# Kernel optimization log

Hardware: AMD Instinct MI355X
Metric: run time of the kernel (lower is better)

## Reference

```python
import jax, jax.numpy as jnp
import numpy as np

B, H, W, F, D = 8, 126, 126, 64, 32
ITERS, NIT = 3, 20
RHO, NU, DT, FRC = 1.0, 0.1, 0.1, 1.0
DX = 2.0 / (B + 1)
DY = 2.0 / (H + 1)
DX2, DY2 = DX * DX, DY * DY
DEN = 2.0 * (DX2 + DY2)


def _b_term(du_dx, dv_dy, du_dy, dv_dx):
    return RHO * ((du_dx + dv_dy) / DT - du_dx**2 - 2.0 * du_dy * dv_dx - dv_dy**2)


def build_b(u, v):
    b = jnp.zeros_like(u)
    # interior
    b = b.at[:, 1:-1, 1:-1].set(_b_term(
        (u[:, 1:-1, 2:] - u[:, 1:-1, :-2]) / (2 * DX),
        (v[:, 2:, 1:-1] - v[:, :-2, 1:-1]) / (2 * DY),
        (u[:, 2:, 1:-1] - u[:, :-2, 1:-1]) / (2 * DY),
        (v[:, 1:-1, 2:] - v[:, 1:-1, :-2]) / (2 * DX)))
    # periodic wrap, last column
    b = b.at[:, 1:-1, -1].set(_b_term(
        (u[:, 1:-1, 0] - u[:, 1:-1, -2]) / (2 * DX),
        (v[:, 2:, -1] - v[:, :-2, -1]) / (2 * DY),
        (u[:, 2:, -1] - u[:, :-2, -1]) / (2 * DY),
        (v[:, 1:-1, 0] - v[:, 1:-1, -2]) / (2 * DX)))
    # periodic wrap, first column
    b = b.at[:, 1:-1, 0].set(_b_term(
        (u[:, 1:-1, 1] - u[:, 1:-1, -1]) / (2 * DX),
        (v[:, 2:, 0] - v[:, :-2, 0]) / (2 * DY),
        (u[:, 2:, 0] - u[:, :-2, 0]) / (2 * DY),
        (v[:, 1:-1, 1] - v[:, 1:-1, -1]) / (2 * DX)))
    return b


def pressure_poisson(p, b):
    c = DX2 * DY2 / DEN

    def step(p, _):
        pn = p
        p = p.at[:, 1:-1, 1:-1].set(
            ((pn[:, 1:-1, 2:] + pn[:, 1:-1, :-2]) * DY2 + (pn[:, 2:, 1:-1] + pn[:, :-2, 1:-1]) * DX2) / DEN
            - c * b[:, 1:-1, 1:-1])
        p = p.at[:, 1:-1, -1].set(
            ((pn[:, 1:-1, 0] + pn[:, 1:-1, -2]) * DY2 + (pn[:, 2:, -1] + pn[:, :-2, -1]) * DX2) / DEN
            - c * b[:, 1:-1, -1])
        p = p.at[:, 1:-1, 0].set(
            ((pn[:, 1:-1, 1] + pn[:, 1:-1, -1]) * DY2 + (pn[:, 2:, 0] + pn[:, :-2, 0]) * DX2) / DEN
            - c * b[:, 1:-1, 0])
        # Neumann-style row boundaries (copy from updated p, as in torch code)
        p = p.at[:, -1].set(p[:, -2])
        p = p.at[:, 0].set(p[:, 1])
        return p, None

    p, _ = jax.lax.scan(step, p, None, length=NIT)
    return p


def velocity_step(u, v, p):
    un, vn = u, v
    uc = un[:, 1:-1, 1:-1]
    vc = vn[:, 1:-1, 1:-1]
    u_i = (uc - uc * DT / DX * (uc - un[:, 1:-1, :-2]) - vc * DT / DY * (uc - un[:, :-2, 1:-1])
           - DT / (2 * RHO * DX) * (p[:, 1:-1, 2:] - p[:, 1:-1, :-2])
           + NU * (DT / DX2 * (un[:, 1:-1, 2:] - 2 * uc + un[:, 1:-1, :-2])
                   + DT / DY2 * (un[:, 2:, 1:-1] - 2 * uc + un[:, :-2, 1:-1]))
           + FRC * DT)
    v_i = (vc - uc * DT / DX * (vc - vn[:, 1:-1, :-2]) - vc * DT / DY * (vc - vn[:, :-2, 1:-1])
           - DT / (2 * RHO * DY) * (p[:, 2:, 1:-1] - p[:, :-2, 1:-1])
           + NU * (DT / DX2 * (vn[:, 1:-1, 2:] - 2 * vc + vn[:, 1:-1, :-2])
                   + DT / DY2 * (vn[:, 2:, 1:-1] - 2 * vc + vn[:, :-2, 1:-1])))
    ue = un[:, 1:-1, -1]
    ve = vn[:, 1:-1, -1]
    u_e = (ue - ue * DT / DX * (ue - un[:, 1:-1, -2]) - ve * DT / DY * (ue - un[:, :-2, -1])
           - DT / (2 * RHO * DX) * (p[:, 1:-1, 0] - p[:, 1:-1, -2])
           + NU * (DT / DX2 * (un[:, 1:-1, 0] - 2 * ue + un[:, 1:-1, -2])
                   + DT / DY2 * (un[:, 2:, -1] - 2 * ue + un[:, :-2, -1]))
           + FRC * DT)
    v_e = (ve - ue * DT / DX * (ve - vn[:, 1:-1, -2]) - ve * DT / DY * (ve - vn[:, :-2, -1])
           - DT / (2 * RHO * DY) * (p[:, 2:, -1] - p[:, :-2, -1])
           + NU * (DT / DX2 * (vn[:, 1:-1, 0] - 2 * ve + vn[:, 1:-1, -2])
                   + DT / DY2 * (vn[:, 2:, -1] - 2 * ve + vn[:, :-2, -1])))
    u0c = un[:, 1:-1, 0]
    v0c = vn[:, 1:-1, 0]
    u_0 = (u0c - u0c * DT / DX * (u0c - un[:, 1:-1, -1]) - v0c * DT / DY * (u0c - un[:, :-2, 0])
           - DT / (2 * RHO * DX) * (p[:, 1:-1, 1] - p[:, 1:-1, -1])
           + NU * (DT / DX2 * (un[:, 1:-1, 1] - 2 * u0c + un[:, 1:-1, -1])
                   + DT / DY2 * (un[:, 2:, 0] - 2 * u0c + un[:, :-2, 0]))
           + FRC * DT)
    v_0 = (v0c - u0c * DT / DX * (v0c - vn[:, 1:-1, -1]) - v0c * DT / DY * (v0c - vn[:, :-2, 0])
           - DT / (2 * RHO * DY) * (p[:, 2:, 0] - p[:, :-2, 0])
           + NU * (DT / DX2 * (vn[:, 1:-1, 1] - 2 * v0c + vn[:, 1:-1, -1])
                   + DT / DY2 * (vn[:, 2:, 0] - 2 * v0c + vn[:, :-2, 0])))
    u = un.at[:, 1:-1, 1:-1].set(u_i).at[:, 1:-1, -1].set(u_e).at[:, 1:-1, 0].set(u_0)
    v = vn.at[:, 1:-1, 1:-1].set(v_i).at[:, 1:-1, -1].set(v_e).at[:, 1:-1, 0].set(v_0)
    u = u.at[:, 0].set(0.0).at[:, -1].set(0.0)
    v = v.at[:, 0].set(0.0).at[:, -1].set(0.0)
    return u, v


def setup_inputs() -> dict:
    key = jax.random.key(0)
    ks = jax.random.split(key, 5)
    x = jax.random.normal(ks[0], (B, H, W, F), jnp.float32) * 0.05
    u0 = jax.random.normal(ks[1], (B, H + 2, W + 2, D), jnp.float32) * 0.05
    v0 = jax.random.normal(ks[2], (B, H + 2, W + 2, D), jnp.float32) * 0.05
    w = jax.random.normal(ks[3], (D, F), jnp.float32) / np.float32(np.sqrt(F))
    b_lin = jax.random.normal(ks[4], (D,), jnp.float32) * 0.01
    return {"x": x, "u0": u0, "v0": v0, "w": w, "b_lin": b_lin}


def reference(x, u0, v0, w, b_lin):
    # pad spatial dims by 1 then linear preprocess: (B,H+2,W+2,F) -> (B,H+2,W+2,D)
    p = jnp.pad(x, ((0, 0), (1, 1), (1, 1), (0, 0)))
    p = jnp.einsum('bhwf,df->bhwd', p, w) + b_lin
    u, v = u0, v0
    for _ in range(ITERS):
        b = build_b(u, v)
        p = pressure_poisson(p, b)
        u, v = velocity_step(u, v, p)
    return p[:, -1, :, :]  # (B, W+2, D)
```

## Files before the change

### kernel.cpp

```cpp
#include <hip/hip_runtime.h>

#define NITER 20
#define OUTER 3

constexpr double DXd  = 2.0 / 9.0;
constexpr double DYd  = 2.0 / 127.0;
constexpr double DX2d = DXd * DXd;
constexpr double DY2d = DYd * DYd;
constexpr double DENd = 2.0 * (DX2d + DY2d);

constexpr float K1     = (float)(DY2d / DENd);
constexpr float K2     = (float)(DX2d / DENd);
constexpr float CC     = (float)(DX2d * DY2d / DENd);
constexpr float INV2DX = (float)(1.0 / (2.0 * DXd));
constexpr float INV2DY = (float)(1.0 / (2.0 * DYd));
constexpr float INVDT  = (float)(1.0 / 0.1);
constexpr float DTDX   = (float)(0.1 / DXd);
constexpr float DTDY   = (float)(0.1 / DYd);
constexpr float PGX    = (float)(0.1 / (2.0 * 1.0 * DXd));
constexpr float PGY    = (float)(0.1 / (2.0 * 1.0 * DYd));
constexpr float A1     = (float)(0.1 / DX2d);
constexpr float A2     = (float)(0.1 / DY2d);
constexpr float NUf    = 0.1f;
constexpr float FDT    = 0.1f;

#define ROR1(x)  __int_as_float(__builtin_amdgcn_mov_dpp(__float_as_int(x), 0x121, 0xF, 0xF, false))
#define ROR15(x) __int_as_float(__builtin_amdgcn_mov_dpp(__float_as_int(x), 0x12F, 0xF, 0xF, false))
#define FROM_LO(x) (selLower ? ROR1(x) : ROR15(x))
#define FROM_HI(x) (selLower ? ROR15(x) : ROR1(x))

__global__ __launch_bounds__(256) void einsum_kernel(
    const float* __restrict__ x, const float* __restrict__ w,
    const float* __restrict__ bl, float* __restrict__ p0)
{
    int id = blockIdx.x * 256 + threadIdx.x;
    int c = id & 127, r = (id >> 7) & 127, b = id >> 14;
    float acc[32];
#pragma unroll
    for (int d = 0; d < 32; ++d) acc[d] = bl[d];
    if (r >= 1 && r <= 126 && c >= 1 && c <= 126) {
        const float* xp = x + (((size_t)(b * 126 + (r - 1))) * 126 + (c - 1)) * 64;
#pragma unroll
        for (int f = 0; f < 64; f += 4) {
            float4 xv = *(const float4*)(xp + f);
#pragma unroll
            for (int d = 0; d < 32; ++d) {
                acc[d] += xv.x * w[d * 64 + f] + xv.y * w[d * 64 + f + 1]
                        + xv.z * w[d * 64 + f + 2] + xv.w * w[d * 64 + f + 3];
            }
        }
    }
    float* op = p0 + ((size_t)b * 32) * 16384 + r * 128 + c;
#pragma unroll
    for (int d = 0; d < 32; ++d) op[(size_t)d * 16384] = acc[d];
}

__global__ __launch_bounds__(512, 2) void sim_kernel(
    const float* __restrict__ u0, const float* __restrict__ v0,
    const float* __restrict__ p0ws, const float* __restrict__ x,
    const float* __restrict__ w, const float* __restrict__ bl,
    float* __restrict__ out, int use_ws)
{
    __shared__ float sP[2][32][2][128];
    __shared__ float sU[32][2][128];
    __shared__ float sV[32][2][128];

    const int tid = threadIdx.x;
    const int tx = tid & 15, ty = tid >> 4;
    const int c0 = tx << 3, r0 = ty << 2;
    const int lane = tid & 63;
    const int bb = blockIdx.x & 7;
    const int d  = blockIdx.x >> 3;
    const int tyN = (ty > 0) ? ty - 1 : 0;
    const int tyS = (ty < 31) ? ty + 1 : 31;

    const int pr = __builtin_amdgcn_mov_dpp(lane, 0x121, 0xF, 0xF, false);
    const bool selLower = (pr == ((lane & 48) | ((lane + 15) & 15)));

    float pC[4][8], uC[4][8], vC[4][8], cb[4][8];

#pragma unroll
    for (int r = 0; r < 4; ++r) {
        const size_t base = ((size_t)((bb * 128 + (r0 + r)) * 128 + c0)) * 32 + d;
#pragma unroll
        for (int c = 0; c < 8; ++c) {
            uC[r][c] = u0[base + (size_t)c * 32];
            vC[r][c] = v0[base + (size_t)c * 32];
        }
    }

    if (use_ws) {
        const float* pp = p0ws + ((size_t)(bb * 32 + d)) * 16384;
#pragma unroll
        for (int r = 0; r < 4; ++r) {
            float4 a = *(const float4*)(pp + (r0 + r) * 128 + c0);
            float4 b = *(const float4*)(pp + (r0 + r) * 128 + c0 + 4);
            pC[r][0] = a.x; pC[r][1] = a.y; pC[r][2] = a.z; pC[r][3] = a.w;
            pC[r][4] = b.x; pC[r][5] = b.y; pC[r][6] = b.z; pC[r][7] = b.w;
        }
    } else {
        const float blv = bl[d];
#pragma unroll
        for (int r = 0; r < 4; ++r) {
            const int gr = r0 + r;
#pragma unroll
            for (int c = 0; c < 8; ++c) {
                const int gc = c0 + c;
                float acc = blv;
                if (gr >= 1 && gr <= 126 && gc >= 1 && gc <= 126) {
                    const float* xp = x + (((size_t)(bb * 126 + (gr - 1))) * 126 + (gc - 1)) * 64;
                    for (int f = 0; f < 64; f += 4) {
                        float4 xv = *(const float4*)(xp + f);
                        acc += xv.x * w[d * 64 + f] + xv.y * w[d * 64 + f + 1]
                             + xv.z * w[d * 64 + f + 2] + xv.w * w[d * 64 + f + 3];
                    }
                }
                pC[r][c] = acc;
            }
        }
    }

    int s = 0;
    *(float4*)&sP[0][ty][0][c0]     = make_float4(pC[0][0], pC[0][1], pC[0][2], pC[0][3]);
    *(float4*)&sP[0][ty][0][c0 + 4] = make_float4(pC[0][4], pC[0][5], pC[0][6], pC[0][7]);
    *(float4*)&sP[0][ty][1][c0]     = make_float4(pC[3][0], pC[3][1], pC[3][2], pC[3][3]);
    *(float4*)&sP[0][ty][1][c0 + 4] = make_float4(pC[3][4], pC[3][5], pC[3][6], pC[3][7]);
    *(float4*)&sU[ty][0][c0]        = make_float4(uC[0][0], uC[0][1], uC[0][2], uC[0][3]);
    *(float4*)&sU[ty][0][c0 + 4]    = make_float4(uC[0][4], uC[0][5], uC[0][6], uC[0][7]);
    *(float4*)&sU[ty][1][c0]        = make_float4(uC[3][0], uC[3][1], uC[3][2], uC[3][3]);
    *(float4*)&sU[ty][1][c0 + 4]    = make_float4(uC[3][4], uC[3][5], uC[3][6], uC[3][7]);
    *(float4*)&sV[ty][0][c0]        = make_float4(vC[0][0], vC[0][1], vC[0][2], vC[0][3]);
    *(float4*)&sV[ty][0][c0 + 4]    = make_float4(vC[0][4], vC[0][5], vC[0][6], vC[0][7]);
    *(float4*)&sV[ty][1][c0]        = make_float4(vC[3][0], vC[3][1], vC[3][2], vC[3][3]);
    *(float4*)&sV[ty][1][c0 + 4]    = make_float4(vC[3][4], vC[3][5], vC[3][6], vC[3][7]);
    __syncthreads();

    for (int outer = 0; outer < OUTER; ++outer) {
        {
            float uNh[8], uSh[8], vNh[8], vSh[8];
            {
                float4 a, b;
                a = *(const float4*)&sU[tyN][1][c0]; b = *(const float4*)&sU[tyN][1][c0 + 4];
                uNh[0]=a.x; uNh[1]=a.y; uNh[2]=a.z; uNh[3]=a.w; uNh[4]=b.x; uNh[5]=b.y; uNh[6]=b.z; uNh[7]=b.w;
                a = *(const float4*)&sU[tyS][0][c0]; b = *(const float4*)&sU[tyS][0][c0 + 4];
                uSh[0]=a.x; uSh[1]=a.y; uSh[2]=a.z; uSh[3]=a.w; uSh[4]=b.x; uSh[5]=b.y; uSh[6]=b.z; uSh[7]=b.w;
                a = *(const float4*)&sV[tyN][1][c0]; b = *(const float4*)&sV[tyN][1][c0 + 4];
                vNh[0]=a.x; vNh[1]=a.y; vNh[2]=a.z; vNh[3]=a.w; vNh[4]=b.x; vNh[5]=b.y; vNh[6]=b.z; vNh[7]=b.w;
                a = *(const float4*)&sV[tyS][0][c0]; b = *(const float4*)&sV[tyS][0][c0 + 4];
                vSh[0]=a.x; vSh[1]=a.y; vSh[2]=a.z; vSh[3]=a.w; vSh[4]=b.x; vSh[5]=b.y; vSh[6]=b.z; vSh[7]=b.w;
            }
#pragma unroll
            for (int r = 0; r < 4; ++r) {
                float uWh = FROM_LO(uC[r][7]);
                float uEh = FROM_HI(uC[r][0]);
                float vWh = FROM_LO(vC[r][7]);
                float vEh = FROM_HI(vC[r][0]);
#pragma unroll
                for (int c = 0; c < 8; ++c) {
                    float uE = (c < 7) ? uC[r][c + 1] : uEh;
                    float uW = (c > 0) ? uC[r][c - 1] : uWh;
                    float vE = (c < 7) ? vC[r][c + 1] : vEh;
                    float vW = (c > 0) ? vC[r][c - 1] : vWh;
                    float uN = (r > 0) ? uC[r - 1][c] : uNh[c];
                    float uS = (r < 3) ? uC[r + 1][c] : uSh[c];
                    float vN = (r > 0) ? vC[r - 1][c] : vNh[c];
                    float vS = (r < 3) ? vC[r + 1][c] : vSh[c];
                    float dudx = (uE - uW) * INV2DX;
                    float dvdy = (vS - vN) * INV2DY;
                    float dudy = (uS - uN) * INV2DY;
                    float dvdx = (vE - vW) * INV2DX;
                    float bt = (dudx + dvdy) * INVDT - dudx * dudx
                             - 2.0f * dudy * dvdx - dvdy * dvdy;
                    cb[r][c] = CC * bt;
                }
            }
        }

        for (int it = 0; it < NITER; ++it) {
            float nrow[8], shalo[8];
            {
                float4 a, b;
                a = *(const float4*)&sP[s][tyN][1][c0]; b = *(const float4*)&sP[s][tyN][1][c0 + 4];
                nrow[0]=a.x; nrow[1]=a.y; nrow[2]=a.z; nrow[3]=a.w; nrow[4]=b.x; nrow[5]=b.y; nrow[6]=b.z; nrow[7]=b.w;
                a = *(const float4*)&sP[s][tyS][0][c0]; b = *(const float4*)&sP[s][tyS][0][c0 + 4];
                shalo[0]=a.x; shalo[1]=a.y; shalo[2]=a.z; shalo[3]=a.w; shalo[4]=b.x; shalo[5]=b.y; shalo[6]=b.z; shalo[7]=b.w;
            }
#pragma unroll
            for (int r = 0; r < 4; ++r) {
                float old0[8];
#pragma unroll
                for (int c = 0; c < 8; ++c) old0[c] = pC[r][c];
                float pWh = FROM_LO(old0[7]);
                float pEh = FROM_HI(old0[0]);
#pragma unroll
                for (int c = 0; c < 8; ++c) {
                    float E = (c < 7) ? old0[c + 1] : pEh;
                    float W = (c > 0) ? old0[c - 1] : pWh;
                    float N = nrow[c];
                    float S = (r < 3) ? pC[r + 1][c] : shalo[c];
                    pC[r][c] = (E + W) * K1 + (N + S) * K2 - cb[r][c];
                }
#pragma unroll
                for (int c = 0; c < 8; ++c) nrow[c] = old0[c];
            }
            if (ty == 0) {
#pragma unroll
                for (int c = 0; c < 8; ++c) pC[0][c] = pC[1][c];
            }
            if (ty == 31) {
#pragma unroll
                for (int c = 0; c < 8; ++c) pC[3][c] = pC[2][c];
            }
            *(float4*)&sP[s ^ 1][ty][0][c0]     = make_float4(pC[0][0], pC[0][1], pC[0][2], pC[0][3]);
            *(float4*)&sP[s ^ 1][ty][0][c0 + 4] = make_float4(pC[0][4], pC[0][5], pC[0][6], pC[0][7]);
            *(float4*)&sP[s ^ 1][ty][1][c0]     = make_float4(pC[3][0], pC[3][1], pC[3][2], pC[3][3]);
            *(float4*)&sP[s ^ 1][ty][1][c0 + 4] = make_float4(pC[3][4], pC[3][5], pC[3][6], pC[3][7]);
            __syncthreads();
            s ^= 1;
        }

        if (outer < OUTER - 1) {
            float uNh[8], uSh[8], vNh[8], vSh[8], pNh[8], pSh[8];
            {
                float4 a, b;
                a = *(const float4*)&sU[tyN][1][c0]; b = *(const float4*)&sU[tyN][1][c0 + 4];
                uNh[0]=a.x; uNh[1]=a.y; uNh[2]=a.z; uNh[3]=a.w; uNh[4]=b.x; uNh[5]=b.y; uNh[6]=b.z; uNh[7]=b.w;
                a = *(const float4*)&sU[tyS][0][c0]; b = *(const float4*)&sU[tyS][0][c0 + 4];
                uSh[0]=a.x; uSh[1]=a.y; uSh[2]=a.z; uSh[3]=a.w; uSh[4]=b.x; uSh[5]=b.y; uSh[6]=b.z; uSh[7]=b.w;
                a = *(const float4*)&sV[tyN][1][c0]; b = *(const float4*)&sV[tyN][1][c0 + 4];
                vNh[0]=a.x; vNh[1]=a.y; vNh[2]=a.z; vNh[3]=a.w; vNh[4]=b.x; vNh[5]=b.y; vNh[6]=b.z; vNh[7]=b.w;
                a = *(const float4*)&sV[tyS][0][c0]; b = *(const float4*)&sV[tyS][0][c0 + 4];
                vSh[0]=a.x; vSh[1]=a.y; vSh[2]=a.z; vSh[3]=a.w; vSh[4]=b.x; vSh[5]=b.y; vSh[6]=b.z; vSh[7]=b.w;
                a = *(const float4*)&sP[s][tyN][1][c0]; b = *(const float4*)&sP[s][tyN][1][c0 + 4];
                pNh[0]=a.x; pNh[1]=a.y; pNh[2]=a.z; pNh[3]=a.w; pNh[4]=b.x; pNh[5]=b.y; pNh[6]=b.z; pNh[7]=b.w;
                a = *(const float4*)&sP[s][tyS][0][c0]; b = *(const float4*)&sP[s][tyS][0][c0 + 4];
                pSh[0]=a.x; pSh[1]=a.y; pSh[2]=a.z; pSh[3]=a.w; pSh[4]=b.x; pSh[5]=b.y; pSh[6]=b.z; pSh[7]=b.w;
            }
            __syncthreads();

            float uNrow[8], vNrow[8];
#pragma unroll
            for (int c = 0; c < 8; ++c) { uNrow[c] = uNh[c]; vNrow[c] = vNh[c]; }
#pragma unroll
            for (int r = 0; r < 4; ++r) {
                float uold[8], vold[8];
#pragma unroll
                for (int c = 0; c < 8; ++c) { uold[c] = uC[r][c]; vold[c] = vC[r][c]; }
                float uWh = FROM_LO(uold[7]);
                float uEh = FROM_HI(uold[0]);
                float vWh = FROM_LO(vold[7]);
                float vEh = FROM_HI(vold[0]);
                float pWh = FROM_LO(pC[r][7]);
                float pEh = FROM_HI(pC[r][0]);
#pragma unroll
                for (int c = 0; c < 8; ++c) {
                    float uc = uold[c], vc = vold[c];
                    float uE = (c < 7) ? uold[c + 1] : uEh;
                    float uW = (c > 0) ? uold[c - 1] : uWh;
                    float vE = (c < 7) ? vold[c + 1] : vEh;
                    float vW = (c > 0) ? vold[c - 1] : vWh;
                    float uN = uNrow[c];
                    float uS = (r < 3) ? uC[r + 1][c] : uSh[c];
                    float vN = vNrow[c];
                    float vS = (r < 3) ? vC[r + 1][c] : vSh[c];
                    float pE = (c < 7) ? pC[r][c + 1] : pEh;
                    float pW = (c > 0) ? pC[r][c - 1] : pWh;
                    float pN = (r > 0) ? pC[r - 1][c] : pNh[c];
                    float pS = (r < 3) ? pC[r + 1][c] : pSh[c];

                    float unew = uc - uc * DTDX * (uc - uW) - vc * DTDY * (uc - uN)
                               - PGX * (pE - pW)
                               + NUf * (A1 * (uE - 2.0f * uc + uW) + A2 * (uS - 2.0f * uc + uN))
                               + FDT;
                    float vnew = vc - uc * DTDX * (vc - vW) - vc * DTDY * (vc - vN)
                               - PGY * (pS - pN)
                               + NUf * (A1 * (vE - 2.0f * vc + vW) + A2 * (vS - 2.0f * vc + vN));
                    uC[r][c] = unew;
                    vC[r][c] = vnew;
                }
#pragma unroll
                for (int c = 0; c < 8; ++c) { uNrow[c] = uold[c]; vNrow[c] = vold[c]; }
            }
            if (ty == 0) {
#pragma unroll
                for (int c = 0; c < 8; ++c) { uC[0][c] = 0.0f; vC[0][c] = 0.0f; }
            }
            if (ty == 31) {
#pragma unroll
                for (int c = 0; c < 8; ++c) { uC[3][c] = 0.0f; vC[3][c] = 0.0f; }
            }
            *(float4*)&sU[ty][0][c0]     = make_float4(uC[0][0], uC[0][1], uC[0][2], uC[0][3]);
            *(float4*)&sU[ty][0][c0 + 4] = make_float4(uC[0][4], uC[0][5], uC[0][6], uC[0][7]);
            *(float4*)&sU[ty][1][c0]     = make_float4(uC[3][0], uC[3][1], uC[3][2], uC[3][3]);
            *(float4*)&sU[ty][1][c0 + 4] = make_float4(uC[3][4], uC[3][5], uC[3][6], uC[3][7]);
            *(float4*)&sV[ty][0][c0]     = make_float4(vC[0][0], vC[0][1], vC[0][2], vC[0][3]);
            *(float4*)&sV[ty][0][c0 + 4] = make_float4(vC[0][4], vC[0][5], vC[0][6], vC[0][7]);
            *(float4*)&sV[ty][1][c0]     = make_float4(vC[3][0], vC[3][1], vC[3][2], vC[3][3]);
            *(float4*)&sV[ty][1][c0 + 4] = make_float4(vC[3][4], vC[3][5], vC[3][6], vC[3][7]);
            __syncthreads();
        }
    }

    if (ty == 31) {
        float* op = out + ((size_t)bb * 128 + c0) * 32 + d;
#pragma unroll
        for (int c = 0; c < 8; ++c) op[(size_t)c * 32] = pC[3][c];
    }
}

extern "C" void kernel_launch(void* const* d_in, const int* in_sizes, int n_in,
                              void* d_out, int out_size, void* d_ws, size_t ws_size,
                              hipStream_t stream) {
    const float* x  = (const float*)d_in[0];
    const float* u0 = (const float*)d_in[1];
    const float* v0 = (const float*)d_in[2];
    const float* w  = (const float*)d_in[3];
    const float* bl = (const float*)d_in[4];
    float* out = (float*)d_out;
    float* p0  = (float*)d_ws;

    const size_t need = (size_t)8 * 32 * 128 * 128 * sizeof(float);
    const int use_ws = (ws_size >= need) ? 1 : 0;

    if (use_ws) {
        einsum_kernel<<<512, 256, 0, stream>>>(x, w, bl, p0);
    }
    sim_kernel<<<256, 512, 0, stream>>>(u0, v0, p0, x, w, bl, out, use_ws);
}
```

Baseline: 282.2 us.

## Keep full u/v fields in shared memory and single-buffer pressure halos

Stores the whole u and v planes in LDS, with a swizzled column layout, instead of holding them in registers, and rebuilds the b-term and velocity updates as rolling row windows read from LDS. The aim is to free about 64 VGPRs per thread and cut LDS bank conflicts. The pressure halo buffer goes from double to single buffering, which adds a second barrier to every Poisson iteration. The larger LDS footprint (about 144KB) likely allows only one block per CU, not the two the launch bounds ask for.

```diff
diff --git a/kernel.cpp b/kernel.cpp
--- a/kernel.cpp
+++ b/kernel.cpp
@@ -29,6 +29,17 @@
 #define FROM_LO(x) (selLower ? ROR1(x) : ROR15(x))
 #define FROM_HI(x) (selLower ? ROR15(x) : ROR1(x))
 
+#define PLOAD(dst, plane, r) do { \
+    float4 _a = *(const float4*)&(plane)[(r) * 128 + (tx << 2)]; \
+    float4 _b = *(const float4*)&(plane)[(r) * 128 + 64 + (tx << 2)]; \
+    (dst)[0]=_a.x; (dst)[1]=_a.y; (dst)[2]=_a.z; (dst)[3]=_a.w; \
+    (dst)[4]=_b.x; (dst)[5]=_b.y; (dst)[6]=_b.z; (dst)[7]=_b.w; } while (0)
+#define PSTORE(plane, r, src) do { \
+    *(float4*)&(plane)[(r) * 128 + (tx << 2)] = make_float4((src)[0],(src)[1],(src)[2],(src)[3]); \
+    *(float4*)&(plane)[(r) * 128 + 64 + (tx << 2)] = make_float4((src)[4],(src)[5],(src)[6],(src)[7]); } while (0)
+#define SLOAD(dst, tyy, slot)  PLOAD(dst, sPm, ((tyy) * 2 + (slot)))
+#define SSTORE(tyy, slot, src) PSTORE(sPm, ((tyy) * 2 + (slot)), src)
+
 __global__ __launch_bounds__(256) void einsum_kernel(
     const float* __restrict__ x, const float* __restrict__ w,
     const float* __restrict__ bl, float* __restrict__ p0)
@@ -61,9 +72,9 @@
     const float* __restrict__ w, const float* __restrict__ bl,
     float* __restrict__ out, int use_ws)
 {
-    __shared__ float sP[2][32][2][128];
-    __shared__ float sU[32][2][128];
-    __shared__ float sV[32][2][128];
+    __shared__ float sU[128 * 128];
+    __shared__ float sV[128 * 128];
+    __shared__ float sPm[32 * 2 * 128];
 
     const int tid = threadIdx.x;
     const int tx = tid & 15, ty = tid >> 4;
@@ -73,20 +84,25 @@
     const int d  = blockIdx.x >> 3;
     const int tyN = (ty > 0) ? ty - 1 : 0;
     const int tyS = (ty < 31) ? ty + 1 : 31;
+    const int rowN = (r0 > 0) ? r0 - 1 : 0;
+    const int rowS = (r0 + 4 < 128) ? r0 + 4 : 127;
 
     const int pr = __builtin_amdgcn_mov_dpp(lane, 0x121, 0xF, 0xF, false);
     const bool selLower = (pr == ((lane & 48) | ((lane + 15) & 15)));
 
-    float pC[4][8], uC[4][8], vC[4][8], cb[4][8];
+    float pC[4][8];
 
 #pragma unroll
     for (int r = 0; r < 4; ++r) {
         const size_t base = ((size_t)((bb * 128 + (r0 + r)) * 128 + c0)) * 32 + d;
+        float ut[8], vt[8];
 #pragma unroll
         for (int c = 0; c < 8; ++c) {
-            uC[r][c] = u0[base + (size_t)c * 32];
-            vC[r][c] = v0[base + (size_t)c * 32];
-        }
+            ut[c] = u0[base + (size_t)c * 32];
+            vt[c] = v0[base + (size_t)c * 32];
+        }
+        PSTORE(sU, r0 + r, ut);
+        PSTORE(sV, r0 + r, vt);
     }
 
     if (use_ws) {
@@ -120,71 +136,50 @@
         }
     }
 
-    int s = 0;
-    *(float4*)&sP[0][ty][0][c0]     = make_float4(pC[0][0], pC[0][1], pC[0][2], pC[0][3]);
-    *(float4*)&sP[0][ty][0][c0 + 4] = make_float4(pC[0][4], pC[0][5], pC[0][6], pC[0][7]);
-    *(float4*)&sP[0][ty][1][c0]     = make_float4(pC[3][0], pC[3][1], pC[3][2], pC[3][3]);
-    *(float4*)&sP[0][ty][1][c0 + 4] = make_float4(pC[3][4], pC[3][5], pC[3][6], pC[3][7]);
-    *(float4*)&sU[ty][0][c0]        = make_float4(uC[0][0], uC[0][1], uC[0][2], uC[0][3]);
-    *(float4*)&sU[ty][0][c0 + 4]    = make_float4(uC[0][4], uC[0][5], uC[0][6], uC[0][7]);
-    *(float4*)&sU[ty][1][c0]        = make_float4(uC[3][0], uC[3][1], uC[3][2], uC[3][3]);
-    *(float4*)&sU[ty][1][c0 + 4]    = make_float4(uC[3][4], uC[3][5], uC[3][6], uC[3][7]);
-    *(float4*)&sV[ty][0][c0]        = make_float4(vC[0][0], vC[0][1], vC[0][2], vC[0][3]);
-    *(float4*)&sV[ty][0][c0 + 4]    = make_float4(vC[0][4], vC[0][5], vC[0][6], vC[0][7]);
-    *(float4*)&sV[ty][1][c0]        = make_float4(vC[3][0], vC[3][1], vC[3][2], vC[3][3]);
-    *(float4*)&sV[ty][1][c0 + 4]    = make_float4(vC[3][4], vC[3][5], vC[3][6], vC[3][7]);
+    SSTORE(ty, 0, pC[0]);
+    SSTORE(ty, 1, pC[3]);
     __syncthreads();
 
     for (int outer = 0; outer < OUTER; ++outer) {
+        float cb[4][8];
         {
-            float uNh[8], uSh[8], vNh[8], vSh[8];
-            {
-                float4 a, b;
-                a = *(const float4*)&sU[tyN][1][c0]; b = *(const float4*)&sU[tyN][1][c0 + 4];
-                uNh[0]=a.x; uNh[1]=a.y; uNh[2]=a.z; uNh[3]=a.w; uNh[4]=b.x; uNh[5]=b.y; uNh[6]=b.z; uNh[7]=b.w;
-                a = *(const float4*)&sU[tyS][0][c0]; b = *(const float4*)&sU[tyS][0][c0 + 4];
-                uSh[0]=a.x; uSh[1]=a.y; uSh[2]=a.z; uSh[3]=a.w; uSh[4]=b.x; uSh[5]=b.y; uSh[6]=b.z; uSh[7]=b.w;
-                a = *(const float4*)&sV[tyN][1][c0]; b = *(const float4*)&sV[tyN][1][c0 + 4];
-                vNh[0]=a.x; vNh[1]=a.y; vNh[2]=a.z; vNh[3]=a.w; vNh[4]=b.x; vNh[5]=b.y; vNh[6]=b.z; vNh[7]=b.w;
-                a = *(const float4*)&sV[tyS][0][c0]; b = *(const float4*)&sV[tyS][0][c0 + 4];
-                vSh[0]=a.x; vSh[1]=a.y; vSh[2]=a.z; vSh[3]=a.w; vSh[4]=b.x; vSh[5]=b.y; vSh[6]=b.z; vSh[7]=b.w;
-            }
+            float um[8], uc[8], up[8], vm[8], vc[8], vp[8];
+            PLOAD(um, sU, rowN); PLOAD(vm, sV, rowN);
+            PLOAD(uc, sU, r0);   PLOAD(vc, sV, r0);
 #pragma unroll
             for (int r = 0; r < 4; ++r) {
-                float uWh = FROM_LO(uC[r][7]);
-                float uEh = FROM_HI(uC[r][0]);
-                float vWh = FROM_LO(vC[r][7]);
-                float vEh = FROM_HI(vC[r][0]);
-#pragma unroll
-                for (int c = 0; c < 8; ++c) {
-                    float uE = (c < 7) ? uC[r][c + 1] : uEh;
-                    float uW = (c > 0) ? uC[r][c - 1] : uWh;
-                    float vE = (c < 7) ? vC[r][c + 1] : vEh;
-                    float vW = (c > 0) ? vC[r][c - 1] : vWh;
-                    float uN = (r > 0) ? uC[r - 1][c] : uNh[c];
-                    float uS = (r < 3) ? uC[r + 1][c] : uSh[c];
-                    float vN = (r > 0) ? vC[r - 1][c] : vNh[c];
-                    float vS = (r < 3) ? vC[r + 1][c] : vSh[c];
+                const int rn = (r < 3) ? (r0 + r + 1) : rowS;
+                PLOAD(up, sU, rn); PLOAD(vp, sV, rn);
+                float uWh = FROM_LO(uc[7]);
+                float uEh = FROM_HI(uc[0]);
+                float vWh = FROM_LO(vc[7]);
+                float vEh = FROM_HI(vc[0]);
+#pragma unroll
+                for (int c = 0; c < 8; ++c) {
+                    float uE = (c < 7) ? uc[c + 1] : uEh;
+                    float uW = (c > 0) ? uc[c - 1] : uWh;
+                    float vE = (c < 7) ? vc[c + 1] : vEh;
+                    float vW = (c > 0) ? vc[c - 1] : vWh;
                     float dudx = (uE - uW) * INV2DX;
-                    float dvdy = (vS - vN) * INV2DY;
-                    float dudy = (uS - uN) * INV2DY;
+                    float dvdy = (vp[c] - vm[c]) * INV2DY;
+                    float dudy = (up[c] - um[c]) * INV2DY;
                     float dvdx = (vE - vW) * INV2DX;
                     float bt = (dudx + dvdy) * INVDT - dudx * dudx
                              - 2.0f * dudy * dvdx - dvdy * dvdy;
                     cb[r][c] = CC * bt;
                 }
+#pragma unroll
+                for (int c = 0; c < 8; ++c) {
+                    um[c] = uc[c]; uc[c] = up[c];
+                    vm[c] = vc[c]; vc[c] = vp[c];
+                }
             }
         }
 
         for (int it = 0; it < NITER; ++it) {
             float nrow[8], shalo[8];
-            {
-                float4 a, b;
-                a = *(const float4*)&sP[s][tyN][1][c0]; b = *(const float4*)&sP[s][tyN][1][c0 + 4];
-                nrow[0]=a.x; nrow[1]=a.y; nrow[2]=a.z; nrow[3]=a.w; nrow[4]=b.x; nrow[5]=b.y; nrow[6]=b.z; nrow[7]=b.w;
-                a = *(const float4*)&sP[s][tyS][0][c0]; b = *(const float4*)&sP[s][tyS][0][c0 + 4];
-                shalo[0]=a.x; shalo[1]=a.y; shalo[2]=a.z; shalo[3]=a.w; shalo[4]=b.x; shalo[5]=b.y; shalo[6]=b.z; shalo[7]=b.w;
-            }
+            SLOAD(nrow, tyN, 1);
+            SLOAD(shalo, tyS, 0);
 #pragma unroll
             for (int r = 0; r < 4; ++r) {
                 float old0[8];
@@ -211,92 +206,76 @@
 #pragma unroll
                 for (int c = 0; c < 8; ++c) pC[3][c] = pC[2][c];
             }
-            *(float4*)&sP[s ^ 1][ty][0][c0]     = make_float4(pC[0][0], pC[0][1], pC[0][2], pC[0][3]);
-            *(float4*)&sP[s ^ 1][ty][0][c0 + 4] = make_float4(pC[0][4], pC[0][5], pC[0][6], pC[0][7]);
-            *(float4*)&sP[s ^ 1][ty][1][c0]     = make_float4(pC[3][0], pC[3][1], pC[3][2], pC[3][3]);
-            *(float4*)&sP[s ^ 1][ty][1][c0 + 4] = make_float4(pC[3][4], pC[3][5], pC[3][6], pC[3][7]);
             __syncthreads();
-            s ^= 1;
+            SSTORE(ty, 0, pC[0]);
+            SSTORE(ty, 1, pC[3]);
+            __syncthreads();
         }
 
         if (outer < OUTER - 1) {
-            float uNh[8], uSh[8], vNh[8], vSh[8], pNh[8], pSh[8];
-            {
-                float4 a, b;
-                a = *(const float4*)&sU[tyN][1][c0]; b = *(const float4*)&sU[tyN][1][c0 + 4];
-                uNh[0]=a.x; uNh[1]=a.y; uNh[2]=a.z; uNh[3]=a.w; uNh[4]=b.x; uNh[5]=b.y; uNh[6]=b.z; uNh[7]=b.w;
-                a = *(const float4*)&sU[tyS][0][c0]; b = *(const float4*)&sU[tyS][0][c0 + 4];
-                uSh[0]=a.x; uSh[1]=a.y; uSh[2]=a.z; uSh[3]=a.w; uSh[4]=b.x; uSh[5]=b.y; uSh[6]=b.z; uSh[7]=b.w;
-                a = *(const float4*)&sV[tyN][1][c0]; b = *(const float4*)&sV[tyN][1][c0 + 4];
-                vNh[0]=a.x; vNh[1]=a.y; vNh[2]=a.z; vNh[3]=a.w; vNh[4]=b.x; vNh[5]=b.y; vNh[6]=b.z; vNh[7]=b.w;
-                a = *(const float4*)&sV[tyS][0][c0]; b = *(const float4*)&sV[tyS][0][c0 + 4];
-                vSh[0]=a.x; vSh[1]=a.y; vSh[2]=a.z; vSh[3]=a.w; vSh[4]=b.x; vSh[5]=b.y; vSh[6]=b.z; vSh[7]=b.w;
-                a = *(const float4*)&sP[s][tyN][1][c0]; b = *(const float4*)&sP[s][tyN][1][c0 + 4];
-                pNh[0]=a.x; pNh[1]=a.y; pNh[2]=a.z; pNh[3]=a.w; pNh[4]=b.x; pNh[5]=b.y; pNh[6]=b.z; pNh[7]=b.w;
-                a = *(const float4*)&sP[s][tyS][0][c0]; b = *(const float4*)&sP[s][tyS][0][c0 + 4];
-                pSh[0]=a.x; pSh[1]=a.y; pSh[2]=a.z; pSh[3]=a.w; pSh[4]=b.x; pSh[5]=b.y; pSh[6]=b.z; pSh[7]=b.w;
-            }
+            float uSh[8], vSh[8], um[8], uc[8], up[8], vm[8], vc[8], vp[8];
+            PLOAD(uSh, sU, rowS); PLOAD(vSh, sV, rowS);
+            PLOAD(um, sU, rowN);  PLOAD(vm, sV, rowN);
+            PLOAD(uc, sU, r0);    PLOAD(vc, sV, r0);
+            PLOAD(up, sU, r0 + 1); PLOAD(vp, sV, r0 + 1);
             __syncthreads();
-
-            float uNrow[8], vNrow[8];
-#pragma unroll
-            for (int c = 0; c < 8; ++c) { uNrow[c] = uNh[c]; vNrow[c] = vNh[c]; }
+            float pNh[8], pSh[8];
+            SLOAD(pNh, tyN, 1);
+            SLOAD(pSh, tyS, 0);
 #pragma unroll
             for (int r = 0; r < 4; ++r) {
-                float uold[8], vold[8];
-#pragma unroll
-                for (int c = 0; c < 8; ++c) { uold[c] = uC[r][c]; vold[c] = vC[r][c]; }
-                float uWh = FROM_LO(uold[7]);
-                float uEh = FROM_HI(uold[0]);
-                float vWh = FROM_LO(vold[7]);
-                float vEh = FROM_HI(vold[0]);
+                float uWh = FROM_LO(uc[7]);
+                float uEh = FROM_HI(uc[0]);
+                float vWh = FROM_LO(vc[7]);
+                float vEh = FROM_HI(vc[0]);
                 float pWh = FROM_LO(pC[r][7]);
                 float pEh = FROM_HI(pC[r][0]);
-#pragma unroll
-                for (int c = 0; c < 8; ++c) {
-                    float uc = uold[c], vc = vold[c];
-                    float uE = (c < 7) ? uold[c + 1] : uEh;
-                    float uW = (c > 0) ? uold[c - 1] : uWh;
-                    float vE = (c < 7) ? vold[c + 1] : vEh;
-                    float vW = (c > 0) ? vold[c - 1] : vWh;
-                    float uN = uNrow[c];
-                    float uS = (r < 3) ? uC[r + 1][c] : uSh[c];
-                    float vN = vNrow[c];
-                    float vS = (r < 3) ? vC[r + 1][c] : vSh[c];
+                float un[8], vn[8];
+#pragma unroll
+                for (int c = 0; c < 8; ++c) {
+                    float ucc = uc[c], vcc = vc[c];
+                    float uE = (c < 7) ? uc[c + 1] : uEh;
+                    float uW = (c > 0) ? uc[c - 1] : uWh;
+                    float vE = (c < 7) ? vc[c + 1] : vEh;
+                    float vW = (c > 0) ? vc[c - 1] : vWh;
+                    float uN = um[c], uS = up[c];
+                    float vN = vm[c], vS = vp[c];
                     float pE = (c < 7) ? pC[r][c + 1] : pEh;
                     float pW = (c > 0) ? pC[r][c - 1] : pWh;
                     float pN = (r > 0) ? pC[r - 1][c] : pNh[c];
                     float pS = (r < 3) ? pC[r + 1][c] : pSh[c];
 
-                    float unew = uc - uc * DTDX * (uc - uW) - vc * DTDY * (uc - uN)
-                               - PGX * (pE - pW)
-                               + NUf * (A1 * (uE - 2.0f * uc + uW) + A2 * (uS - 2.0f * uc + uN))
-                               + FDT;
-                    float vnew = vc - uc * DTDX * (vc - vW) - vc * DTDY * (vc - vN)
-                               - PGY * (pS - pN)
-                               + NUf * (A1 * (vE - 2.0f * vc + vW) + A2 * (vS - 2.0f * vc + vN));
-                    uC[r][c] = unew;
-                    vC[r][c] = vnew;
-                }
-#pragma unroll
-                for (int c = 0; c < 8; ++c) { uNrow[c] = uold[c]; vNrow[c] = vold[c]; }
-            }
-            if (ty == 0) {
-#pragma unroll
-                for (int c = 0; c < 8; ++c) { uC[0][c] = 0.0f; vC[0][c] = 0.0f; }
-            }
-            if (ty == 31) {
-#pragma unroll
-                for (int c = 0; c < 8; ++c) { uC[3][c] = 0.0f; vC[3][c] = 0.0f; }
-            }
-            *(float4*)&sU[ty][0][c0]     = make_float4(uC[0][0], uC[0][1], uC[0][2], uC[0][3]);
-            *(float4*)&sU[ty][0][c0 + 4] = make_float4(uC[0][4], uC[0][5], uC[0][6], uC[0][7]);
-            *(float4*)&sU[ty][1][c0]     = make_float4(uC[3][0], uC[3][1], uC[3][2], uC[3][3]);
-            *(float4*)&sU[ty][1][c0 + 4] = make_float4(uC[3][4], uC[3][5], uC[3][6], uC[3][7]);
-            *(float4*)&sV[ty][0][c0]     = make_float4(vC[0][0], vC[0][1], vC[0][2], vC[0][3]);
-            *(float4*)&sV[ty][0][c0 + 4] = make_float4(vC[0][4], vC[0][5], vC[0][6], vC[0][7]);
-            *(float4*)&sV[ty][1][c0]     = make_float4(vC[3][0], vC[3][1], vC[3][2], vC[3][3]);
-            *(float4*)&sV[ty][1][c0 + 4] = make_float4(vC[3][4], vC[3][5], vC[3][6], vC[3][7]);
+                    un[c] = ucc - ucc * DTDX * (ucc - uW) - vcc * DTDY * (ucc - uN)
+                          - PGX * (pE - pW)
+                          + NUf * (A1 * (uE - 2.0f * ucc + uW) + A2 * (uS - 2.0f * ucc + uN))
+                          + FDT;
+                    vn[c] = vcc - ucc * DTDX * (vcc - vW) - vcc * DTDY * (vcc - vN)
+                          - PGY * (pS - pN)
+                          + NUf * (A1 * (vE - 2.0f * vcc + vW) + A2 * (vS - 2.0f * vcc + vN));
+                }
+                if (ty == 0 && r == 0) {
+#pragma unroll
+                    for (int c = 0; c < 8; ++c) { un[c] = 0.0f; vn[c] = 0.0f; }
+                }
+                if (ty == 31 && r == 3) {
+#pragma unroll
+                    for (int c = 0; c < 8; ++c) { un[c] = 0.0f; vn[c] = 0.0f; }
+                }
+                PSTORE(sU, r0 + r, un);
+                PSTORE(sV, r0 + r, vn);
+#pragma unroll
+                for (int c = 0; c < 8; ++c) {
+                    um[c] = uc[c]; uc[c] = up[c];
+                    vm[c] = vc[c]; vc[c] = vp[c];
+                }
+                if (r < 2) {
+                    PLOAD(up, sU, r0 + r + 2);
+                    PLOAD(vp, sV, r0 + r + 2);
+                } else if (r == 2) {
+#pragma unroll
+                    for (int c = 0; c < 8; ++c) { up[c] = uSh[c]; vp[c] = vSh[c]; }
+                }
+            }
             __syncthreads();
         }
     }
```

After: 249.3 us. -11.7%, faster.
